# Kernel tuning notes

Hardware: AMD Instinct MI355X
Metric: run time of the kernel (lower is better)

## Reference

```python
import jax, jax.numpy as jnp
import numpy as np

NUM_CODES = 1024
CODE_DIM = 256
EMA_DECAY = 0.99
COMMITMENT = 0.25
EPS = 1e-6


def setup_inputs() -> dict:
    key = jax.random.key(0)
    k1, k2 = jax.random.split(key)
    z = jax.random.normal(k1, (64, 512, CODE_DIM), dtype=jnp.float32)
    embedding = jax.random.normal(k2, (NUM_CODES, CODE_DIM), dtype=jnp.float32)
    cluster_size = jnp.zeros((NUM_CODES,), dtype=jnp.float32)
    embedding_avg = embedding.copy()
    return {"z": z, "embedding": embedding, "cluster_size": cluster_size,
            "embedding_avg": embedding_avg}


def reference(z, embedding, cluster_size, embedding_avg):
    K, D = embedding.shape
    flat = z.reshape(-1, D)                                  # [N, D]
    dist = (jnp.sum(flat * flat, axis=1, keepdims=True)
            - 2.0 * (flat @ embedding.T)
            + jnp.sum(embedding * embedding, axis=1))
    indices = jnp.argmin(dist, axis=1)                       # [N]
    z_q = embedding[indices].reshape(z.shape)

    # EMA codebook update (training branch, no-grad in original)
    counts = jax.ops.segment_sum(jnp.ones_like(indices, dtype=flat.dtype),
                                 indices, num_segments=K)    # one-hot col sums
    embed_sum = jax.ops.segment_sum(flat, indices, num_segments=K)  # [K, D]
    new_cluster_size = cluster_size * EMA_DECAY + (1.0 - EMA_DECAY) * counts
    new_embedding_avg = embedding_avg * EMA_DECAY + (1.0 - EMA_DECAY) * embed_sum
    n = jnp.sum(new_cluster_size)
    cs = (new_cluster_size + EPS) / (n + K * EPS)
    new_embedding = new_embedding_avg / cs[:, None]

    loss = COMMITMENT * jnp.mean((jax.lax.stop_gradient(z_q) - z) ** 2)
    z_q_st = z + jax.lax.stop_gradient(z_q - z)
    return (z_q_st, loss, indices, new_cluster_size, new_embedding_avg,
            new_embedding)
```

## Files before the change

### kernel.cpp

```cpp
#include <hip/hip_runtime.h>

#define N_ROWS   32768
#define KCODES   1024
#define DDIM     256
#define RPB      64
#define NBLK     512

#define O_ZQ     0
#define O_LOSS   8388608
#define O_IDX    8388609
#define O_NCS    8421377
#define O_NEA    8422401
#define O_NEMB   8684545

#define W_ESUM   0
#define W_CNT    262144
#define W_ENORM  263168
#define W_LOSSP  264192
#define W_CUR    264704
#define W_N      265728
#define W_IDX    265792
#define W_SORT   298560

typedef _Float16 half_t;
typedef __attribute__((ext_vector_type(8))) _Float16 half8;
typedef __attribute__((ext_vector_type(4))) float floatx4;

__global__ __launch_bounds__(256)
void k_prep2(const float* __restrict__ emb, float* __restrict__ enorm,
             half_t* __restrict__ Bp, float* __restrict__ zero_ws) {
    __shared__ half_t hi[16 * 256];
    __shared__ half_t lo[16 * 256];
    __shared__ float  ssum[256];
    const int ct  = blockIdx.x;
    const int tid = threadIdx.x;
    const int c16 = tid >> 4;
    const int dp  = tid & 15;

    {
        float4 z4 = {0.f, 0.f, 0.f, 0.f};
        float4* wsf4 = (float4*)zero_ws;
        int t = ct * 256 + tid;
        #pragma unroll
        for (int i = 0; i < 4; ++i) wsf4[t + i * 16384] = z4;
        if (t < 256) wsf4[65536 + t] = z4;
    }

    float ss = 0.f;
    #pragma unroll
    for (int i = 0; i < 4; ++i) {
        float4 v = *(const float4*)(emb + (size_t)(ct * 16 + c16) * DDIM + dp * 16 + i * 4);
        ss += v.x * v.x + v.y * v.y + v.z * v.z + v.w * v.w;
        #pragma unroll
        for (int q = 0; q < 4; ++q) {
            float f = (&v.x)[q];
            half_t h = (half_t)f;
            hi[c16 * 256 + dp * 16 + i * 4 + q] = h;
            lo[c16 * 256 + dp * 16 + i * 4 + q] = (half_t)(f - (float)h);
        }
    }
    ssum[tid] = ss;
    __syncthreads();
    if (tid < 16) {
        float s = 0.f;
        #pragma unroll
        for (int i = 0; i < 16; ++i) s += ssum[tid * 16 + i];
        enorm[ct * 16 + tid] = s;
    }

    const int g16 = ((ct >> 4) << 2) | ((ct >> 2) & 3);
    const int ns  = ct & 3;
    #pragma unroll
    for (int i = 0; i < 4; ++i) {
        int f    = tid + i * 256;
        int ks   = f >> 6;
        int lane = f & 63;
        int cc   = lane & 15;
        int seg  = ks >> 3;
        int ko   = (ks & 7) * 32 + (lane >> 4) * 8;
        const half_t* src = (seg == 1) ? lo : hi;
        half8 v = *(const half8*)(src + cc * 256 + ko);
        *(half8*)(Bp + (((size_t)(g16 * 16 + ks) * 4 + ns) * 64 + lane) * 8) = v;
    }
}

__global__ __launch_bounds__(512)
void k_argmin(const float* __restrict__ z, const half_t* __restrict__ Bp,
              const float* __restrict__ enorm, const float* __restrict__ embf,
              int* __restrict__ out_idx, float* __restrict__ out_idx_f,
              float* __restrict__ out_zq, float* __restrict__ lossp,
              int* __restrict__ counts_i) {
    __shared__ __align__(16) half_t As[RPB * 512];

    const int tid  = threadIdx.x;
    const int w    = tid >> 6;
    const int lane = tid & 63;
    const int tx   = lane & 15;
    const int quad = lane >> 4;
    const int rh   = w >> 2;
    const int cq   = w & 3;
    const int rbase = blockIdx.x * RPB;

    #pragma unroll
    for (int it = 0; it < 4; ++it) {
        int f   = tid + it * 512;
        int row = f >> 5;
        int g   = f & 31;
        const float* zp = z + (size_t)(rbase + row) * DDIM + g * 8;
        float4 v0 = *(const float4*)zp;
        float4 v1 = *(const float4*)(zp + 4);
        half8 hi, lo;
        hi[0] = (half_t)v0.x; lo[0] = (half_t)(v0.x - (float)hi[0]);
        hi[1] = (half_t)v0.y; lo[1] = (half_t)(v0.y - (float)hi[1]);
        hi[2] = (half_t)v0.z; lo[2] = (half_t)(v0.z - (float)hi[2]);
        hi[3] = (half_t)v0.w; lo[3] = (half_t)(v0.w - (float)hi[3]);
        hi[4] = (half_t)v1.x; lo[4] = (half_t)(v1.x - (float)hi[4]);
        hi[5] = (half_t)v1.y; lo[5] = (half_t)(v1.y - (float)hi[5]);
        hi[6] = (half_t)v1.z; lo[6] = (half_t)(v1.z - (float)hi[6]);
        hi[7] = (half_t)v1.w; lo[7] = (half_t)(v1.w - (float)hi[7]);
        int sw = row & 7;
        *(half8*)(&As[row * 512 + ((g ^ sw)) * 8])        = hi;
        *(half8*)(&As[row * 512 + (((32 + g) ^ sw)) * 8]) = lo;
    }
    __syncthreads();

    floatx4 zero4 = {0.f, 0.f, 0.f, 0.f};
    float bd[2][4];
    int   bi[2][4];
    #pragma unroll
    for (int mt = 0; mt < 2; ++mt)
        #pragma unroll
        for (int r = 0; r < 4; ++r) { bd[mt][r] = 3.402823466e38f; bi[mt][r] = 0; }

    for (int g4 = 0; g4 < 4; ++g4) {
        const int cb = cq * 256 + g4 * 64;
        const half_t* Bg = Bp + (size_t)(cq * 4 + g4) * 32768 + (size_t)lane * 8;

        floatx4 acc[2][4];
        #pragma unroll
        for (int mt = 0; mt < 2; ++mt)
            #pragma unroll
            for (int ns = 0; ns < 4; ++ns) acc[mt][ns] = zero4;

        half8 B0[4], B1[4];
        #define LOADB(PK, BUF)                                                 \
            { const half_t* bp_ = Bg + (PK) * 2048;                            \
              _Pragma("unroll")                                                \
              for (int ns = 0; ns < 4; ++ns)                                   \
                  BUF[ns] = *(const half8*)(bp_ + ns * 512); }
        #define MFMA_BLK(BUF)                                                  \
            _Pragma("unroll")                                                  \
            for (int mt = 0; mt < 2; ++mt)                                     \
                _Pragma("unroll")                                              \
                for (int ns = 0; ns < 4; ++ns)                                 \
                    acc[mt][ns] = __builtin_amdgcn_mfma_f32_16x16x32_f16(      \
                        a[mt], BUF[ns], acc[mt][ns], 0, 0, 0);

        LOADB(0, B0);
        LOADB(1, B1);

        #pragma unroll 2
        for (int ks = 0; ks < 24; ++ks) {
            const int k8b = ((ks & 16) << 1) + (ks & 7) * 4;
            half8 a[2];
            #pragma unroll
            for (int mt = 0; mt < 2; ++mt) {
                int row = rh * 32 + mt * 16 + tx;
                a[mt] = *(half8*)(&As[row * 512 + ((k8b + quad) ^ (row & 7)) * 8]);
            }
            if (ks & 1) { MFMA_BLK(B1) } else { MFMA_BLK(B0) }
            if (ks + 2 < 24) {
                const int pkp = (ks + 2) & 15;
                if (ks & 1) { LOADB(pkp, B1); } else { LOADB(pkp, B0); }
            }
        }
        #undef LOADB
        #undef MFMA_BLK

        #pragma unroll
        for (int ns = 0; ns < 4; ++ns) {
            float en = enorm[cb + ns * 16 + tx];
            int   cc = cb + ns * 16 + tx;
            #pragma unroll
            for (int mt = 0; mt < 2; ++mt)
                #pragma unroll
                for (int r = 0; r < 4; ++r) {
                    float d = fmaf(-2.f, acc[mt][ns][r], en);
                    if (d < bd[mt][r]) { bd[mt][r] = d; bi[mt][r] = cc; }
                }
        }
    }

    #pragma unroll
    for (int mt = 0; mt < 2; ++mt)
        #pragma unroll
        for (int r = 0; r < 4; ++r) {
            float d = bd[mt][r];
            int   b = bi[mt][r];
            #pragma unroll
            for (int off = 8; off > 0; off >>= 1) {
                float od = __shfl_xor(d, off);
                int   ob = __shfl_xor(b, off);
                if (od < d || (od == d && ob < b)) { d = od; b = ob; }
            }
            bd[mt][r] = d; bi[mt][r] = b;
        }

    __syncthreads();
    float* sd   = (float*)As;
    int*   si   = ((int*)As) + 256;
    int*   sidx = ((int*)As) + 512;
    if (tx == 0) {
        #pragma unroll
        for (int mt = 0; mt < 2; ++mt)
            #pragma unroll
            for (int r = 0; r < 4; ++r) {
                int row = rh * 32 + mt * 16 + quad * 4 + r;
                sd[row * 4 + cq] = bd[mt][r];
                si[row * 4 + cq] = bi[mt][r];
            }
    }
    __syncthreads();
    if (tid < RPB) {
        int row = tid;
        float d = sd[row * 4];
        int   b = si[row * 4];
        #pragma unroll
        for (int ww = 1; ww < 4; ++ww) {
            float od = sd[row * 4 + ww];
            int   ob = si[row * 4 + ww];
            if (od < d || (od == d && ob < b)) { d = od; b = ob; }
        }
        sidx[row] = b;
        out_idx[rbase + row]   = b;
        out_idx_f[rbase + row] = (float)b;
        atomicAdd(&counts_i[b], 1);
    }
    __syncthreads();

    float l = 0.f;
    #pragma unroll
    for (int u = 0; u < 8; ++u) {
        int gi  = tid + u * 512;
        int row = gi >> 6;
        int c4  = gi & 63;
        int k   = sidx[row];
        float4 zv = *(const float4*)(z    + (size_t)(rbase + row) * DDIM + c4 * 4);
        float4 ev = *(const float4*)(embf + (size_t)k * DDIM + c4 * 4);
        float dx = ev.x - zv.x, dy = ev.y - zv.y, dz = ev.z - zv.z, dw = ev.w - zv.w;
        float4 o = { zv.x + dx, zv.y + dy, zv.z + dz, zv.w + dw };
        *(float4*)(out_zq + (size_t)(rbase + row) * DDIM + c4 * 4) = o;
        l += dx * dx + dy * dy + dz * dz + dw * dw;
    }
    #pragma unroll
    for (int off = 32; off > 0; off >>= 1) l += __shfl_down(l, off);
    __shared__ float ls[8];
    if (lane == 0) ls[w] = l;
    __syncthreads();
    if (tid == 0) {
        float s = 0.f;
        #pragma unroll
        for (int i = 0; i < 8; ++i) s += ls[i];
        lossp[blockIdx.x] = s;
    }
}

__global__ __launch_bounds__(256)
void k_scan(const float* __restrict__ cs_in, const int* __restrict__ counts_i,
            const float* __restrict__ lossp, float* __restrict__ out_ncs,
            int* __restrict__ cursors,
            float* __restrict__ n_out, float* __restrict__ loss_out) {
    const int tid = threadIdx.x;
    __shared__ int ps[256];
    int c[4]; int pt = 0;
    #pragma unroll
    for (int i = 0; i < 4; ++i) { c[i] = counts_i[tid * 4 + i]; pt += c[i]; }
    ps[tid] = pt;
    __syncthreads();
    for (int s = 1; s < 256; s <<= 1) {
        int v = (tid >= s) ? ps[tid - s] : 0;
        __syncthreads();
        ps[tid] += v;
        __syncthreads();
    }
    int o = ps[tid] - pt;
    float v = 0.f;
    #pragma unroll
    for (int i = 0; i < 4; ++i) {
        cursors[tid * 4 + i] = o;
        o += c[i];
        float nc = cs_in[tid * 4 + i] * 0.99f + 0.01f * (float)c[i];
        out_ncs[tid * 4 + i] = nc;
        v += nc;
    }
    float l = 0.f;
    for (int i = tid; i < NBLK; i += 256) l += lossp[i];
    #pragma unroll
    for (int off = 32; off > 0; off >>= 1) {
        v += __shfl_down(v, off);
        l += __shfl_down(l, off);
    }
    __shared__ float sv[4], sl[4];
    if ((tid & 63) == 0) { sv[tid >> 6] = v; sl[tid >> 6] = l; }
    __syncthreads();
    if (tid == 0) {
        n_out[0]    = sv[0] + sv[1] + sv[2] + sv[3];
        loss_out[0] = 0.25f * ((sl[0] + sl[1] + sl[2] + sl[3]) / 8388608.0f);
    }
}

__global__ __launch_bounds__(256)
void k_rank(const int* __restrict__ idx, int* __restrict__ cursors,
            int* __restrict__ rows_sorted) {
    int r = blockIdx.x * 256 + threadIdx.x;
    int k = idx[r];
    int pos = atomicAdd(&cursors[k], 1);
    rows_sorted[pos] = r;
}

__global__ __launch_bounds__(256)
void k_esum2(const float* __restrict__ z, const int* __restrict__ rows_sorted,
             const int* __restrict__ idx, float* __restrict__ esum) {
    const int tid  = threadIdx.x;
    const int w    = tid >> 6;
    const int lane = tid & 63;
    const int base = (blockIdx.x * 4 + w) * 32;

    int r = rows_sorted[base + (lane & 31)];
    int c = idx[r];
    float4 acc = {0.f, 0.f, 0.f, 0.f};
    #pragma unroll 8
    for (int j = 0; j < 32; ++j) {
        int rj = __shfl(r, j);
        int cj = __shfl(c, j);
        float4 zv = *(const float4*)(z + (size_t)rj * DDIM + lane * 4);
        acc.x += zv.x; acc.y += zv.y; acc.z += zv.z; acc.w += zv.w;
        int cn = (j < 31) ? __shfl(c, j + 1) : -1;
        if (cn != cj) {
            float* p = esum + (size_t)cj * DDIM + lane * 4;
            atomicAdd(p + 0, acc.x);
            atomicAdd(p + 1, acc.y);
            atomicAdd(p + 2, acc.z);
            atomicAdd(p + 3, acc.w);
            acc.x = 0.f; acc.y = 0.f; acc.z = 0.f; acc.w = 0.f;
        }
    }
}

__global__ __launch_bounds__(256)
void k_embed(const float* __restrict__ ea, const float* __restrict__ esum,
             const float* __restrict__ ncs, const float* __restrict__ n_ws,
             float* __restrict__ out_nea, float* __restrict__ out_nemb) {
    int k = blockIdx.x;
    int d = threadIdx.x;
    size_t off = (size_t)k * DDIM + d;
    float nea = ea[off] * 0.99f + 0.01f * esum[off];
    out_nea[off] = nea;
    float cs = (ncs[k] + 1e-6f) / (n_ws[0] + 0.001024f);
    out_nemb[off] = nea / cs;
}

extern "C" void kernel_launch(void* const* d_in, const int* in_sizes, int n_in,
                              void* d_out, int out_size, void* d_ws, size_t ws_size,
                              hipStream_t stream) {
    const float* z   = (const float*)d_in[0];
    const float* emb = (const float*)d_in[1];
    const float* cs  = (const float*)d_in[2];
    const float* ea  = (const float*)d_in[3];
    float* out = (float*)d_out;
    float* ws  = (float*)d_ws;

    float* esum    = ws + W_ESUM;
    int*   cnts    = (int*)(ws + W_CNT);
    float* enorm   = ws + W_ENORM;
    float* lossp   = ws + W_LOSSP;
    int*   curs    = (int*)(ws + W_CUR);
    float* wn      = ws + W_N;
    int*   widx    = (int*)(ws + W_IDX);
    int*   rsorted = (int*)(ws + W_SORT);

    half_t* Bp = (half_t*)(out + O_NEA + 3);

    k_prep2  <<<64, 256, 0, stream>>>(emb, enorm, Bp, ws);
    k_argmin <<<NBLK, 512, 0, stream>>>(z, Bp, enorm, emb,
                                        widx, out + O_IDX, out + O_ZQ, lossp, cnts);
    k_scan   <<<1, 256, 0, stream>>>(cs, cnts, lossp, out + O_NCS, curs,
                                     wn, out + O_LOSS);
    k_rank   <<<N_ROWS / 256, 256, 0, stream>>>(widx, curs, rsorted);
    k_esum2  <<<256, 256, 0, stream>>>(z, rsorted, widx, esum);
    k_embed  <<<KCODES, 256, 0, stream>>>(ea, esum, out + O_NCS, wn,
                                          out + O_NEA, out + O_NEMB);
}
```

Before: 202.1 us.

## Fuse scan, rank, esum and embed into one cooperative kernel

Merges the four post-argmin kernels into a single cooperative-launch kernel that uses grid syncs. Bucket ranks are now taken from the argmin counting atomics, which removes the separate rank pass, and the esum zeroing moves into the tail kernel. Two smaller changes ride along: the argmin kernel gets a remapped z staging load and triple-buffered B prefetch instead of double-buffered. The aim is to cut kernel launch gaps and the serial single-block scan, at the cost of grid-sync overhead and extra register pressure.

```diff
diff --git a/kernel.cpp b/kernel.cpp
--- a/kernel.cpp
+++ b/kernel.cpp
@@ -1,4 +1,7 @@
 #include <hip/hip_runtime.h>
+#include <hip/hip_cooperative_groups.h>
+
+namespace cg = cooperative_groups;
 
 #define N_ROWS   32768
 #define KCODES   1024
@@ -21,6 +24,7 @@
 #define W_N      265728
 #define W_IDX    265792
 #define W_SORT   298560
+#define W_RANK   331328
 
 typedef _Float16 half_t;
 typedef __attribute__((ext_vector_type(8))) _Float16 half8;
@@ -28,7 +32,7 @@
 
 __global__ __launch_bounds__(256)
 void k_prep2(const float* __restrict__ emb, float* __restrict__ enorm,
-             half_t* __restrict__ Bp, float* __restrict__ zero_ws) {
+             half_t* __restrict__ Bp, int* __restrict__ cnts) {
     __shared__ half_t hi[16 * 256];
     __shared__ half_t lo[16 * 256];
     __shared__ float  ssum[256];
@@ -37,13 +41,9 @@
     const int c16 = tid >> 4;
     const int dp  = tid & 15;
 
-    {
-        float4 z4 = {0.f, 0.f, 0.f, 0.f};
-        float4* wsf4 = (float4*)zero_ws;
-        int t = ct * 256 + tid;
-        #pragma unroll
-        for (int i = 0; i < 4; ++i) wsf4[t + i * 16384] = z4;
-        if (t < 256) wsf4[65536 + t] = z4;
+    if (ct == 0) {
+        int4 zz = {0, 0, 0, 0};
+        ((int4*)cnts)[tid] = zz;
     }
 
     float ss = 0.f;
@@ -89,7 +89,7 @@
               const float* __restrict__ enorm, const float* __restrict__ embf,
               int* __restrict__ out_idx, float* __restrict__ out_idx_f,
               float* __restrict__ out_zq, float* __restrict__ lossp,
-              int* __restrict__ counts_i) {
+              int* __restrict__ counts_i, int* __restrict__ rank_ws) {
     __shared__ __align__(16) half_t As[RPB * 512];
 
     const int tid  = threadIdx.x;
@@ -101,26 +101,27 @@
     const int cq   = w & 3;
     const int rbase = blockIdx.x * RPB;
 
-    #pragma unroll
-    for (int it = 0; it < 4; ++it) {
-        int f   = tid + it * 512;
-        int row = f >> 5;
-        int g   = f & 31;
-        const float* zp = z + (size_t)(rbase + row) * DDIM + g * 8;
-        float4 v0 = *(const float4*)zp;
-        float4 v1 = *(const float4*)(zp + 4);
-        half8 hi, lo;
-        hi[0] = (half_t)v0.x; lo[0] = (half_t)(v0.x - (float)hi[0]);
-        hi[1] = (half_t)v0.y; lo[1] = (half_t)(v0.y - (float)hi[1]);
-        hi[2] = (half_t)v0.z; lo[2] = (half_t)(v0.z - (float)hi[2]);
-        hi[3] = (half_t)v0.w; lo[3] = (half_t)(v0.w - (float)hi[3]);
-        hi[4] = (half_t)v1.x; lo[4] = (half_t)(v1.x - (float)hi[4]);
-        hi[5] = (half_t)v1.y; lo[5] = (half_t)(v1.y - (float)hi[5]);
-        hi[6] = (half_t)v1.z; lo[6] = (half_t)(v1.z - (float)hi[6]);
-        hi[7] = (half_t)v1.w; lo[7] = (half_t)(v1.w - (float)hi[7]);
-        int sw = row & 7;
-        *(half8*)(&As[row * 512 + ((g ^ sw)) * 8])        = hi;
-        *(half8*)(&As[row * 512 + (((32 + g) ^ sw)) * 8]) = lo;
+    {
+        const int arow = w * 8 + (lane >> 3);
+        const int sw   = arow & 7;
+        #pragma unroll
+        for (int it = 0; it < 4; ++it) {
+            int g = it * 8 + (lane & 7);
+            const float* zp = z + (size_t)(rbase + arow) * DDIM + g * 8;
+            float4 v0 = *(const float4*)zp;
+            float4 v1 = *(const float4*)(zp + 4);
+            half8 hi, lo;
+            hi[0] = (half_t)v0.x; lo[0] = (half_t)(v0.x - (float)hi[0]);
+            hi[1] = (half_t)v0.y; lo[1] = (half_t)(v0.y - (float)hi[1]);
+            hi[2] = (half_t)v0.z; lo[2] = (half_t)(v0.z - (float)hi[2]);
+            hi[3] = (half_t)v0.w; lo[3] = (half_t)(v0.w - (float)hi[3]);
+            hi[4] = (half_t)v1.x; lo[4] = (half_t)(v1.x - (float)hi[4]);
+            hi[5] = (half_t)v1.y; lo[5] = (half_t)(v1.y - (float)hi[5]);
+            hi[6] = (half_t)v1.z; lo[6] = (half_t)(v1.z - (float)hi[6]);
+            hi[7] = (half_t)v1.w; lo[7] = (half_t)(v1.w - (float)hi[7]);
+            *(half8*)(&As[arow * 512 + ((g ^ sw)) * 8])        = hi;
+            *(half8*)(&As[arow * 512 + (((32 + g) ^ sw)) * 8]) = lo;
+        }
     }
     __syncthreads();
 
@@ -142,7 +143,7 @@
             #pragma unroll
             for (int ns = 0; ns < 4; ++ns) acc[mt][ns] = zero4;
 
-        half8 B0[4], B1[4];
+        half8 B0[4], B1[4], B2[4];
         #define LOADB(PK, BUF)                                                 \
             { const half_t* bp_ = Bg + (PK) * 2048;                            \
               _Pragma("unroll")                                                \
@@ -158,8 +159,9 @@
 
         LOADB(0, B0);
         LOADB(1, B1);
-
-        #pragma unroll 2
+        LOADB(2, B2);
+
+        #pragma unroll 3
         for (int ks = 0; ks < 24; ++ks) {
             const int k8b = ((ks & 16) << 1) + (ks & 7) * 4;
             half8 a[2];
@@ -168,10 +170,16 @@
                 int row = rh * 32 + mt * 16 + tx;
                 a[mt] = *(half8*)(&As[row * 512 + ((k8b + quad) ^ (row & 7)) * 8]);
             }
-            if (ks & 1) { MFMA_BLK(B1) } else { MFMA_BLK(B0) }
-            if (ks + 2 < 24) {
-                const int pkp = (ks + 2) & 15;
-                if (ks & 1) { LOADB(pkp, B1); } else { LOADB(pkp, B0); }
+            const int m3 = ks % 3;
+            if (m3 == 0) {
+                MFMA_BLK(B0)
+                if (ks + 3 < 24) { LOADB((ks + 3) & 15, B0); }
+            } else if (m3 == 1) {
+                MFMA_BLK(B1)
+                if (ks + 3 < 24) { LOADB((ks + 3) & 15, B1); }
+            } else {
+                MFMA_BLK(B2)
+                if (ks + 3 < 24) { LOADB((ks + 3) & 15, B2); }
             }
         }
         #undef LOADB
@@ -234,7 +242,8 @@
         sidx[row] = b;
         out_idx[rbase + row]   = b;
         out_idx_f[rbase + row] = (float)b;
-        atomicAdd(&counts_i[b], 1);
+        int rk = atomicAdd(&counts_i[b], 1);
+        rank_ws[rbase + row] = rk;
     }
     __syncthreads();
 
@@ -266,12 +275,26 @@
 }
 
 __global__ __launch_bounds__(256)
-void k_scan(const float* __restrict__ cs_in, const int* __restrict__ counts_i,
-            const float* __restrict__ lossp, float* __restrict__ out_ncs,
-            int* __restrict__ cursors,
-            float* __restrict__ n_out, float* __restrict__ loss_out) {
+void k_tail(const float* __restrict__ cs_in, const int* __restrict__ counts_i,
+            const float* __restrict__ lossp, const int* __restrict__ idx,
+            const int* __restrict__ rank_ws, const float* __restrict__ z,
+            const float* __restrict__ ea,
+            float* __restrict__ out_ncs, float* __restrict__ n_ws,
+            float* __restrict__ loss_out, int* __restrict__ rows_sorted,
+            float* __restrict__ esum, float* __restrict__ out_nea,
+            float* __restrict__ out_nemb) {
+    cg::grid_group grid = cg::this_grid();
     const int tid = threadIdx.x;
+    const int bid = blockIdx.x;
+
     __shared__ int ps[256];
+    __shared__ int base_s[1024];
+    __shared__ float sv[4], sl[4];
+
+    {
+        float4 z4 = {0.f, 0.f, 0.f, 0.f};
+        ((float4*)esum)[bid * 256 + tid] = z4;
+    }
     int c[4]; int pt = 0;
     #pragma unroll
     for (int i = 0; i < 4; ++i) { c[i] = counts_i[tid * 4 + i]; pt += c[i]; }
@@ -287,77 +310,78 @@
     float v = 0.f;
     #pragma unroll
     for (int i = 0; i < 4; ++i) {
-        cursors[tid * 4 + i] = o;
+        base_s[tid * 4 + i] = o;
         o += c[i];
-        float nc = cs_in[tid * 4 + i] * 0.99f + 0.01f * (float)c[i];
-        out_ncs[tid * 4 + i] = nc;
-        v += nc;
-    }
-    float l = 0.f;
-    for (int i = tid; i < NBLK; i += 256) l += lossp[i];
-    #pragma unroll
-    for (int off = 32; off > 0; off >>= 1) {
-        v += __shfl_down(v, off);
-        l += __shfl_down(l, off);
-    }
-    __shared__ float sv[4], sl[4];
-    if ((tid & 63) == 0) { sv[tid >> 6] = v; sl[tid >> 6] = l; }
-    __syncthreads();
-    if (tid == 0) {
-        n_out[0]    = sv[0] + sv[1] + sv[2] + sv[3];
-        loss_out[0] = 0.25f * ((sl[0] + sl[1] + sl[2] + sl[3]) / 8388608.0f);
-    }
-}
-
-__global__ __launch_bounds__(256)
-void k_rank(const int* __restrict__ idx, int* __restrict__ cursors,
-            int* __restrict__ rows_sorted) {
-    int r = blockIdx.x * 256 + threadIdx.x;
-    int k = idx[r];
-    int pos = atomicAdd(&cursors[k], 1);
-    rows_sorted[pos] = r;
-}
-
-__global__ __launch_bounds__(256)
-void k_esum2(const float* __restrict__ z, const int* __restrict__ rows_sorted,
-             const int* __restrict__ idx, float* __restrict__ esum) {
-    const int tid  = threadIdx.x;
-    const int w    = tid >> 6;
-    const int lane = tid & 63;
-    const int base = (blockIdx.x * 4 + w) * 32;
-
-    int r = rows_sorted[base + (lane & 31)];
-    int c = idx[r];
-    float4 acc = {0.f, 0.f, 0.f, 0.f};
-    #pragma unroll 8
-    for (int j = 0; j < 32; ++j) {
-        int rj = __shfl(r, j);
-        int cj = __shfl(c, j);
-        float4 zv = *(const float4*)(z + (size_t)rj * DDIM + lane * 4);
-        acc.x += zv.x; acc.y += zv.y; acc.z += zv.z; acc.w += zv.w;
-        int cn = (j < 31) ? __shfl(c, j + 1) : -1;
-        if (cn != cj) {
-            float* p = esum + (size_t)cj * DDIM + lane * 4;
-            atomicAdd(p + 0, acc.x);
-            atomicAdd(p + 1, acc.y);
-            atomicAdd(p + 2, acc.z);
-            atomicAdd(p + 3, acc.w);
-            acc.x = 0.f; acc.y = 0.f; acc.z = 0.f; acc.w = 0.f;
-        }
-    }
-}
-
-__global__ __launch_bounds__(256)
-void k_embed(const float* __restrict__ ea, const float* __restrict__ esum,
-             const float* __restrict__ ncs, const float* __restrict__ n_ws,
-             float* __restrict__ out_nea, float* __restrict__ out_nemb) {
-    int k = blockIdx.x;
-    int d = threadIdx.x;
-    size_t off = (size_t)k * DDIM + d;
-    float nea = ea[off] * 0.99f + 0.01f * esum[off];
-    out_nea[off] = nea;
-    float cs = (ncs[k] + 1e-6f) / (n_ws[0] + 0.001024f);
-    out_nemb[off] = nea / cs;
+        if (bid == 0) {
+            float nc = cs_in[tid * 4 + i] * 0.99f + 0.01f * (float)c[i];
+            out_ncs[tid * 4 + i] = nc;
+            v += nc;
+        }
+    }
+    if (bid == 0) {
+        float l = 0.f;
+        for (int i = tid; i < NBLK; i += 256) l += lossp[i];
+        #pragma unroll
+        for (int off = 32; off > 0; off >>= 1) {
+            v += __shfl_down(v, off);
+            l += __shfl_down(l, off);
+        }
+        if ((tid & 63) == 0) { sv[tid >> 6] = v; sl[tid >> 6] = l; }
+        __syncthreads();
+        if (tid == 0) {
+            n_ws[0]     = sv[0] + sv[1] + sv[2] + sv[3];
+            loss_out[0] = 0.25f * ((sl[0] + sl[1] + sl[2] + sl[3]) / 8388608.0f);
+        }
+    }
+    __syncthreads();
+    if (tid < 128) {
+        int r = bid * 128 + tid;
+        int k = idx[r];
+        rows_sorted[base_s[k] + rank_ws[r]] = r;
+    }
+
+    grid.sync();
+
+    {
+        const int w    = tid >> 6;
+        const int lane = tid & 63;
+        const int base = (bid * 4 + w) * 32;
+        int r = rows_sorted[base + (lane & 31)];
+        int cc = idx[r];
+        float4 acc = {0.f, 0.f, 0.f, 0.f};
+        #pragma unroll 8
+        for (int j = 0; j < 32; ++j) {
+            int rj = __shfl(r, j);
+            int cj = __shfl(cc, j);
+            float4 zv = *(const float4*)(z + (size_t)rj * DDIM + lane * 4);
+            acc.x += zv.x; acc.y += zv.y; acc.z += zv.z; acc.w += zv.w;
+            int cn = (j < 31) ? __shfl(cc, j + 1) : -1;
+            if (cn != cj) {
+                float* p = esum + (size_t)cj * DDIM + lane * 4;
+                atomicAdd(p + 0, acc.x);
+                atomicAdd(p + 1, acc.y);
+                atomicAdd(p + 2, acc.z);
+                atomicAdd(p + 3, acc.w);
+                acc.x = 0.f; acc.y = 0.f; acc.z = 0.f; acc.w = 0.f;
+            }
+        }
+    }
+
+    grid.sync();
+
+    {
+        float nv = n_ws[0];
+        #pragma unroll
+        for (int i = 0; i < 4; ++i) {
+            int k = bid * 4 + i;
+            size_t off = (size_t)k * DDIM + tid;
+            float nea = ea[off] * 0.99f + 0.01f * esum[off];
+            out_nea[off] = nea;
+            float ncv = cs_in[k] * 0.99f + 0.01f * (float)counts_i[k];
+            float csv = (ncv + 1e-6f) / (nv + 0.001024f);
+            out_nemb[off] = nea / csv;
+        }
+    }
 }
 
 extern "C" void kernel_launch(void* const* d_in, const int* in_sizes, int n_in,
@@ -374,20 +398,28 @@
     int*   cnts    = (int*)(ws + W_CNT);
     float* enorm   = ws + W_ENORM;
     float* lossp   = ws + W_LOSSP;
-    int*   curs    = (int*)(ws + W_CUR);
     float* wn      = ws + W_N;
     int*   widx    = (int*)(ws + W_IDX);
     int*   rsorted = (int*)(ws + W_SORT);
+    int*   rankw   = (int*)(ws + W_RANK);
 
     half_t* Bp = (half_t*)(out + O_NEA + 3);
 
-    k_prep2  <<<64, 256, 0, stream>>>(emb, enorm, Bp, ws);
+    k_prep2  <<<64, 256, 0, stream>>>(emb, enorm, Bp, cnts);
     k_argmin <<<NBLK, 512, 0, stream>>>(z, Bp, enorm, emb,
-                                        widx, out + O_IDX, out + O_ZQ, lossp, cnts);
-    k_scan   <<<1, 256, 0, stream>>>(cs, cnts, lossp, out + O_NCS, curs,
-                                     wn, out + O_LOSS);
-    k_rank   <<<N_ROWS / 256, 256, 0, stream>>>(widx, curs, rsorted);
-    k_esum2  <<<256, 256, 0, stream>>>(z, rsorted, widx, esum);
-    k_embed  <<<KCODES, 256, 0, stream>>>(ea, esum, out + O_NCS, wn,
-                                          out + O_NEA, out + O_NEMB);
+                                        widx, out + O_IDX, out + O_ZQ, lossp,
+                                        cnts, rankw);
+
+    float* o_ncs  = out + O_NCS;
+    float* o_loss = out + O_LOSS;
+    float* o_nea  = out + O_NEA;
+    float* o_nemb = out + O_NEMB;
+    void* args[] = {
+        (void*)&cs, (void*)&cnts, (void*)&lossp, (void*)&widx, (void*)&rankw,
+        (void*)&z, (void*)&ea,
+        (void*)&o_ncs, (void*)&wn, (void*)&o_loss, (void*)&rsorted,
+        (void*)&esum, (void*)&o_nea, (void*)&o_nemb
+    };
+    hipLaunchCooperativeKernel((const void*)k_tail, dim3(256), dim3(256),
+                               args, 0, stream);
 }
```

Result: slower. 260.2 us (+28.8%).

## Fuse EMA tail into one atomic-free per-code gather kernel and restructure argmin k-loop

Applied to the files above, without the earlier changes.

Replaces the scan, rank, atomic segment-sum and embed kernels with a single kernel. Each block owns four codes, scans all indices to build a shared-memory list of its rows, and accumulates the z rows in registers without global atomics. This removes three launches and the zeroing of the large esum workspace. The argmin k-loop is also restructured to load the hi and lo A fragments together against the same B buffer, and the A staging is remapped to whole-row ownership per wave. The cost is that every block rereads the full index array, and rows are gathered with little parallelism when a code is popular.

```diff
diff --git a/kernel.cpp b/kernel.cpp
--- a/kernel.cpp
+++ b/kernel.cpp
@@ -13,14 +13,10 @@
 #define O_NEA    8422401
 #define O_NEMB   8684545
 
-#define W_ESUM   0
 #define W_CNT    262144
 #define W_ENORM  263168
 #define W_LOSSP  264192
-#define W_CUR    264704
-#define W_N      265728
 #define W_IDX    265792
-#define W_SORT   298560
 
 typedef _Float16 half_t;
 typedef __attribute__((ext_vector_type(8))) _Float16 half8;
@@ -28,7 +24,7 @@
 
 __global__ __launch_bounds__(256)
 void k_prep2(const float* __restrict__ emb, float* __restrict__ enorm,
-             half_t* __restrict__ Bp, float* __restrict__ zero_ws) {
+             half_t* __restrict__ Bp, int* __restrict__ cnts) {
     __shared__ half_t hi[16 * 256];
     __shared__ half_t lo[16 * 256];
     __shared__ float  ssum[256];
@@ -37,13 +33,9 @@
     const int c16 = tid >> 4;
     const int dp  = tid & 15;
 
-    {
-        float4 z4 = {0.f, 0.f, 0.f, 0.f};
-        float4* wsf4 = (float4*)zero_ws;
-        int t = ct * 256 + tid;
-        #pragma unroll
-        for (int i = 0; i < 4; ++i) wsf4[t + i * 16384] = z4;
-        if (t < 256) wsf4[65536 + t] = z4;
+    if (ct == 0) {
+        int4 zz = {0, 0, 0, 0};
+        ((int4*)cnts)[tid] = zz;
     }
 
     float ss = 0.f;
@@ -101,26 +93,27 @@
     const int cq   = w & 3;
     const int rbase = blockIdx.x * RPB;
 
-    #pragma unroll
-    for (int it = 0; it < 4; ++it) {
-        int f   = tid + it * 512;
-        int row = f >> 5;
-        int g   = f & 31;
-        const float* zp = z + (size_t)(rbase + row) * DDIM + g * 8;
-        float4 v0 = *(const float4*)zp;
-        float4 v1 = *(const float4*)(zp + 4);
-        half8 hi, lo;
-        hi[0] = (half_t)v0.x; lo[0] = (half_t)(v0.x - (float)hi[0]);
-        hi[1] = (half_t)v0.y; lo[1] = (half_t)(v0.y - (float)hi[1]);
-        hi[2] = (half_t)v0.z; lo[2] = (half_t)(v0.z - (float)hi[2]);
-        hi[3] = (half_t)v0.w; lo[3] = (half_t)(v0.w - (float)hi[3]);
-        hi[4] = (half_t)v1.x; lo[4] = (half_t)(v1.x - (float)hi[4]);
-        hi[5] = (half_t)v1.y; lo[5] = (half_t)(v1.y - (float)hi[5]);
-        hi[6] = (half_t)v1.z; lo[6] = (half_t)(v1.z - (float)hi[6]);
-        hi[7] = (half_t)v1.w; lo[7] = (half_t)(v1.w - (float)hi[7]);
-        int sw = row & 7;
-        *(half8*)(&As[row * 512 + ((g ^ sw)) * 8])        = hi;
-        *(half8*)(&As[row * 512 + (((32 + g) ^ sw)) * 8]) = lo;
+    {
+        const int arow = w * 8 + (lane >> 3);
+        const int sw   = arow & 7;
+        #pragma unroll
+        for (int it = 0; it < 4; ++it) {
+            int g = it * 8 + (lane & 7);
+            const float* zp = z + (size_t)(rbase + arow) * DDIM + g * 8;
+            float4 v0 = *(const float4*)zp;
+            float4 v1 = *(const float4*)(zp + 4);
+            half8 hi, lo;
+            hi[0] = (half_t)v0.x; lo[0] = (half_t)(v0.x - (float)hi[0]);
+            hi[1] = (half_t)v0.y; lo[1] = (half_t)(v0.y - (float)hi[1]);
+            hi[2] = (half_t)v0.z; lo[2] = (half_t)(v0.z - (float)hi[2]);
+            hi[3] = (half_t)v0.w; lo[3] = (half_t)(v0.w - (float)hi[3]);
+            hi[4] = (half_t)v1.x; lo[4] = (half_t)(v1.x - (float)hi[4]);
+            hi[5] = (half_t)v1.y; lo[5] = (half_t)(v1.y - (float)hi[5]);
+            hi[6] = (half_t)v1.z; lo[6] = (half_t)(v1.z - (float)hi[6]);
+            hi[7] = (half_t)v1.w; lo[7] = (half_t)(v1.w - (float)hi[7]);
+            *(half8*)(&As[arow * 512 + ((g ^ sw)) * 8])        = hi;
+            *(half8*)(&As[arow * 512 + (((32 + g) ^ sw)) * 8]) = lo;
+        }
     }
     __syncthreads();
 
@@ -148,31 +141,41 @@
               _Pragma("unroll")                                                \
               for (int ns = 0; ns < 4; ++ns)                                   \
                   BUF[ns] = *(const half8*)(bp_ + ns * 512); }
-        #define MFMA_BLK(BUF)                                                  \
+        #define MFMA_BLK(AF, BUF)                                              \
             _Pragma("unroll")                                                  \
             for (int mt = 0; mt < 2; ++mt)                                     \
                 _Pragma("unroll")                                              \
                 for (int ns = 0; ns < 4; ++ns)                                 \
                     acc[mt][ns] = __builtin_amdgcn_mfma_f32_16x16x32_f16(      \
-                        a[mt], BUF[ns], acc[mt][ns], 0, 0, 0);
+                        AF[mt], BUF[ns], acc[mt][ns], 0, 0, 0);
 
         LOADB(0, B0);
         LOADB(1, B1);
 
         #pragma unroll 2
-        for (int ks = 0; ks < 24; ++ks) {
-            const int k8b = ((ks & 16) << 1) + (ks & 7) * 4;
-            half8 a[2];
+        for (int s = 0; s < 8; ++s) {
+            half8 a0[2], a1[2];
             #pragma unroll
             for (int mt = 0; mt < 2; ++mt) {
                 int row = rh * 32 + mt * 16 + tx;
-                a[mt] = *(half8*)(&As[row * 512 + ((k8b + quad) ^ (row & 7)) * 8]);
+                int sw  = row & 7;
+                a0[mt] = *(half8*)(&As[row * 512 + ((s * 4 + quad) ^ sw) * 8]);
+                a1[mt] = *(half8*)(&As[row * 512 + ((32 + s * 4 + quad) ^ sw) * 8]);
             }
-            if (ks & 1) { MFMA_BLK(B1) } else { MFMA_BLK(B0) }
-            if (ks + 2 < 24) {
-                const int pkp = (ks + 2) & 15;
-                if (ks & 1) { LOADB(pkp, B1); } else { LOADB(pkp, B0); }
+            if (s & 1) { MFMA_BLK(a0, B1) MFMA_BLK(a1, B1) LOADB(s + 2, B1); }
+            else       { MFMA_BLK(a0, B0) MFMA_BLK(a1, B0) LOADB(s + 2, B0); }
+        }
+        #pragma unroll 2
+        for (int s = 8; s < 16; ++s) {
+            half8 a0[2];
+            #pragma unroll
+            for (int mt = 0; mt < 2; ++mt) {
+                int row = rh * 32 + mt * 16 + tx;
+                int sw  = row & 7;
+                a0[mt] = *(half8*)(&As[row * 512 + (((s - 8) * 4 + quad) ^ sw) * 8]);
             }
+            if (s & 1) { MFMA_BLK(a0, B1) if (s + 2 < 16) LOADB(s + 2, B1); }
+            else       { MFMA_BLK(a0, B0) if (s + 2 < 16) LOADB(s + 2, B0); }
         }
         #undef LOADB
         #undef MFMA_BLK
@@ -266,98 +269,101 @@
 }
 
 __global__ __launch_bounds__(256)
-void k_scan(const float* __restrict__ cs_in, const int* __restrict__ counts_i,
-            const float* __restrict__ lossp, float* __restrict__ out_ncs,
-            int* __restrict__ cursors,
-            float* __restrict__ n_out, float* __restrict__ loss_out) {
-    const int tid = threadIdx.x;
-    __shared__ int ps[256];
-    int c[4]; int pt = 0;
-    #pragma unroll
-    for (int i = 0; i < 4; ++i) { c[i] = counts_i[tid * 4 + i]; pt += c[i]; }
-    ps[tid] = pt;
-    __syncthreads();
-    for (int s = 1; s < 256; s <<= 1) {
-        int v = (tid >= s) ? ps[tid - s] : 0;
-        __syncthreads();
-        ps[tid] += v;
-        __syncthreads();
-    }
-    int o = ps[tid] - pt;
-    float v = 0.f;
-    #pragma unroll
-    for (int i = 0; i < 4; ++i) {
-        cursors[tid * 4 + i] = o;
-        o += c[i];
-        float nc = cs_in[tid * 4 + i] * 0.99f + 0.01f * (float)c[i];
-        out_ncs[tid * 4 + i] = nc;
-        v += nc;
-    }
-    float l = 0.f;
-    for (int i = tid; i < NBLK; i += 256) l += lossp[i];
-    #pragma unroll
-    for (int off = 32; off > 0; off >>= 1) {
-        v += __shfl_down(v, off);
-        l += __shfl_down(l, off);
-    }
-    __shared__ float sv[4], sl[4];
-    if ((tid & 63) == 0) { sv[tid >> 6] = v; sl[tid >> 6] = l; }
-    __syncthreads();
-    if (tid == 0) {
-        n_out[0]    = sv[0] + sv[1] + sv[2] + sv[3];
-        loss_out[0] = 0.25f * ((sl[0] + sl[1] + sl[2] + sl[3]) / 8388608.0f);
-    }
-}
-
-__global__ __launch_bounds__(256)
-void k_rank(const int* __restrict__ idx, int* __restrict__ cursors,
-            int* __restrict__ rows_sorted) {
-    int r = blockIdx.x * 256 + threadIdx.x;
-    int k = idx[r];
-    int pos = atomicAdd(&cursors[k], 1);
-    rows_sorted[pos] = r;
-}
-
-__global__ __launch_bounds__(256)
-void k_esum2(const float* __restrict__ z, const int* __restrict__ rows_sorted,
-             const int* __restrict__ idx, float* __restrict__ esum) {
+void k_tail2(const float* __restrict__ cs_in, const int* __restrict__ counts_i,
+             const float* __restrict__ lossp, const int* __restrict__ idx,
+             const float* __restrict__ z, const float* __restrict__ ea,
+             float* __restrict__ out_ncs, float* __restrict__ loss_out,
+             float* __restrict__ out_nea, float* __restrict__ out_nemb) {
     const int tid  = threadIdx.x;
+    const int bid  = blockIdx.x;
+    const int kb   = bid * 4;
     const int w    = tid >> 6;
     const int lane = tid & 63;
-    const int base = (blockIdx.x * 4 + w) * 32;
-
-    int r = rows_sorted[base + (lane & 31)];
-    int c = idx[r];
-    float4 acc = {0.f, 0.f, 0.f, 0.f};
-    #pragma unroll 8
-    for (int j = 0; j < 32; ++j) {
-        int rj = __shfl(r, j);
-        int cj = __shfl(c, j);
-        float4 zv = *(const float4*)(z + (size_t)rj * DDIM + lane * 4);
-        acc.x += zv.x; acc.y += zv.y; acc.z += zv.z; acc.w += zv.w;
-        int cn = (j < 31) ? __shfl(c, j + 1) : -1;
-        if (cn != cj) {
-            float* p = esum + (size_t)cj * DDIM + lane * 4;
-            atomicAdd(p + 0, acc.x);
-            atomicAdd(p + 1, acc.y);
-            atomicAdd(p + 2, acc.z);
-            atomicAdd(p + 3, acc.w);
-            acc.x = 0.f; acc.y = 0.f; acc.z = 0.f; acc.w = 0.f;
-        }
-    }
-}
-
-__global__ __launch_bounds__(256)
-void k_embed(const float* __restrict__ ea, const float* __restrict__ esum,
-             const float* __restrict__ ncs, const float* __restrict__ n_ws,
-             float* __restrict__ out_nea, float* __restrict__ out_nemb) {
-    int k = blockIdx.x;
-    int d = threadIdx.x;
-    size_t off = (size_t)k * DDIM + d;
-    float nea = ea[off] * 0.99f + 0.01f * esum[off];
-    out_nea[off] = nea;
-    float cs = (ncs[k] + 1e-6f) / (n_ws[0] + 0.001024f);
-    out_nemb[off] = nea / cs;
+
+    __shared__ int    list[4096];
+    __shared__ int    lcnt;
+    __shared__ float4 accW[4][4][64];
+    __shared__ float  snv[4], slv[4];
+
+    float pn = 0.f;
+    #pragma unroll
+    for (int i = 0; i < 4; ++i) {
+        int c = tid * 4 + i;
+        float nc = cs_in[c] * 0.99f + 0.01f * (float)counts_i[c];
+        pn += nc;
+        if (bid == 0) out_ncs[c] = nc;
+    }
+    float pl = (bid == 0) ? (lossp[tid] + lossp[tid + 256]) : 0.f;
+    #pragma unroll
+    for (int off = 32; off > 0; off >>= 1) {
+        pn += __shfl_down(pn, off);
+        pl += __shfl_down(pl, off);
+    }
+    if (lane == 0) { snv[w] = pn; slv[w] = pl; }
+    __syncthreads();
+    const float nval = snv[0] + snv[1] + snv[2] + snv[3];
+    if (bid == 0 && tid == 0)
+        loss_out[0] = 0.25f * ((slv[0] + slv[1] + slv[2] + slv[3]) / 8388608.0f);
+
+    float4 a0 = {0.f,0.f,0.f,0.f}, a1 = a0, a2 = a0, a3 = a0;
+    for (int ch = 0; ch < 8; ++ch) {
+        __syncthreads();
+        if (tid == 0) lcnt = 0;
+        __syncthreads();
+        const int4* ip = (const int4*)(idx + ch * 4096);
+        #pragma unroll
+        for (int i = 0; i < 4; ++i) {
+            int4 v = ip[tid + i * 256];
+            int r0 = ch * 4096 + (tid + i * 256) * 4;
+            int d;
+            d = v.x - kb; if ((unsigned)d < 4u) { int p = atomicAdd(&lcnt, 1); list[p] = r0 | (d << 15); }
+            d = v.y - kb; if ((unsigned)d < 4u) { int p = atomicAdd(&lcnt, 1); list[p] = (r0 + 1) | (d << 15); }
+            d = v.z - kb; if ((unsigned)d < 4u) { int p = atomicAdd(&lcnt, 1); list[p] = (r0 + 2) | (d << 15); }
+            d = v.w - kb; if ((unsigned)d < 4u) { int p = atomicAdd(&lcnt, 1); list[p] = (r0 + 3) | (d << 15); }
+        }
+        __syncthreads();
+        const int n = lcnt;
+        for (int i = w; i < n; i += 4) {
+            int packed = list[i];
+            int row = packed & 32767;
+            int lc  = packed >> 15;
+            float4 v = *((const float4*)(z + (size_t)row * DDIM) + lane);
+            if      (lc == 0) { a0.x += v.x; a0.y += v.y; a0.z += v.z; a0.w += v.w; }
+            else if (lc == 1) { a1.x += v.x; a1.y += v.y; a1.z += v.z; a1.w += v.w; }
+            else if (lc == 2) { a2.x += v.x; a2.y += v.y; a2.z += v.z; a2.w += v.w; }
+            else              { a3.x += v.x; a3.y += v.y; a3.z += v.z; a3.w += v.w; }
+        }
+    }
+    __syncthreads();
+    accW[0][w][lane] = a0;
+    accW[1][w][lane] = a1;
+    accW[2][w][lane] = a2;
+    accW[3][w][lane] = a3;
+    __syncthreads();
+
+    {
+        const int c = tid >> 6;
+        const int l = tid & 63;
+        float4 e0 = accW[c][0][l];
+        float4 e1 = accW[c][1][l];
+        float4 e2 = accW[c][2][l];
+        float4 e3 = accW[c][3][l];
+        float ex = e0.x + e1.x + e2.x + e3.x;
+        float ey = e0.y + e1.y + e2.y + e3.y;
+        float ez = e0.z + e1.z + e2.z + e3.z;
+        float ew = e0.w + e1.w + e2.w + e3.w;
+        size_t off = (size_t)(kb + c) * DDIM + l * 4;
+        float4 av = *(const float4*)(ea + off);
+        float4 nea = { av.x * 0.99f + 0.01f * ex,
+                       av.y * 0.99f + 0.01f * ey,
+                       av.z * 0.99f + 0.01f * ez,
+                       av.w * 0.99f + 0.01f * ew };
+        *(float4*)(out_nea + off) = nea;
+        float ncv = cs_in[kb + c] * 0.99f + 0.01f * (float)counts_i[kb + c];
+        float csv = (ncv + 1e-6f) / (nval + 0.001024f);
+        float4 nemb = { nea.x / csv, nea.y / csv, nea.z / csv, nea.w / csv };
+        *(float4*)(out_nemb + off) = nemb;
+    }
 }
 
 extern "C" void kernel_launch(void* const* d_in, const int* in_sizes, int n_in,
@@ -370,24 +376,18 @@
     float* out = (float*)d_out;
     float* ws  = (float*)d_ws;
 
-    float* esum    = ws + W_ESUM;
     int*   cnts    = (int*)(ws + W_CNT);
     float* enorm   = ws + W_ENORM;
     float* lossp   = ws + W_LOSSP;
-    int*   curs    = (int*)(ws + W_CUR);
-    float* wn      = ws + W_N;
     int*   widx    = (int*)(ws + W_IDX);
-    int*   rsorted = (int*)(ws + W_SORT);
 
     half_t* Bp = (half_t*)(out + O_NEA + 3);
 
-    k_prep2  <<<64, 256, 0, stream>>>(emb, enorm, Bp, ws);
+    k_prep2  <<<64, 256, 0, stream>>>(emb, enorm, Bp, cnts);
     k_argmin <<<NBLK, 512, 0, stream>>>(z, Bp, enorm, emb,
-                                        widx, out + O_IDX, out + O_ZQ, lossp, cnts);
-    k_scan   <<<1, 256, 0, stream>>>(cs, cnts, lossp, out + O_NCS, curs,
-                                     wn, out + O_LOSS);
-    k_rank   <<<N_ROWS / 256, 256, 0, stream>>>(widx, curs, rsorted);
-    k_esum2  <<<256, 256, 0, stream>>>(z, rsorted, widx, esum);
-    k_embed  <<<KCODES, 256, 0, stream>>>(ea, esum, out + O_NCS, wn,
-                                          out + O_NEA, out + O_NEMB);
+                                        widx, out + O_IDX, out + O_ZQ, lossp,
+                                        cnts);
+    k_tail2  <<<256, 256, 0, stream>>>(cs, cnts, lossp, widx, z, ea,
+                                       out + O_NCS, out + O_LOSS,
+                                       out + O_NEA, out + O_NEMB);
 }
```

Result: slower. 270.0 us (+33.6%).

## Fuse scan and rank into one scatter kernel, reuse A fragments in argmin

Applied to the files above, without the earlier changes.

The argmin kernel now records each row's atomic rank within its code bucket. That lets a new multi-block scatter kernel compute prefix offsets per block and place rows without a second round of atomics, merging the single-block scan and the rank kernel into one launch. The MFMA K-loop is restructured to load B fragments for 16 steps instead of 24 and reuse them across hi and lo A halves, and the z staging loop is remapped per warp. The embed kernel is vectorised to float4 with 4 codes per block. The trade-off is that every block redundantly recomputes the 1024-entry prefix scan, and the rank buffer costs extra workspace.

```diff
diff --git a/kernel.cpp b/kernel.cpp
--- a/kernel.cpp
+++ b/kernel.cpp
@@ -17,10 +17,10 @@
 #define W_CNT    262144
 #define W_ENORM  263168
 #define W_LOSSP  264192
-#define W_CUR    264704
 #define W_N      265728
 #define W_IDX    265792
 #define W_SORT   298560
+#define W_RANK   331328
 
 typedef _Float16 half_t;
 typedef __attribute__((ext_vector_type(8))) _Float16 half8;
@@ -89,7 +89,7 @@
               const float* __restrict__ enorm, const float* __restrict__ embf,
               int* __restrict__ out_idx, float* __restrict__ out_idx_f,
               float* __restrict__ out_zq, float* __restrict__ lossp,
-              int* __restrict__ counts_i) {
+              int* __restrict__ counts_i, int* __restrict__ rank_ws) {
     __shared__ __align__(16) half_t As[RPB * 512];
 
     const int tid  = threadIdx.x;
@@ -101,26 +101,27 @@
     const int cq   = w & 3;
     const int rbase = blockIdx.x * RPB;
 
-    #pragma unroll
-    for (int it = 0; it < 4; ++it) {
-        int f   = tid + it * 512;
-        int row = f >> 5;
-        int g   = f & 31;
-        const float* zp = z + (size_t)(rbase + row) * DDIM + g * 8;
-        float4 v0 = *(const float4*)zp;
-        float4 v1 = *(const float4*)(zp + 4);
-        half8 hi, lo;
-        hi[0] = (half_t)v0.x; lo[0] = (half_t)(v0.x - (float)hi[0]);
-        hi[1] = (half_t)v0.y; lo[1] = (half_t)(v0.y - (float)hi[1]);
-        hi[2] = (half_t)v0.z; lo[2] = (half_t)(v0.z - (float)hi[2]);
-        hi[3] = (half_t)v0.w; lo[3] = (half_t)(v0.w - (float)hi[3]);
-        hi[4] = (half_t)v1.x; lo[4] = (half_t)(v1.x - (float)hi[4]);
-        hi[5] = (half_t)v1.y; lo[5] = (half_t)(v1.y - (float)hi[5]);
-        hi[6] = (half_t)v1.z; lo[6] = (half_t)(v1.z - (float)hi[6]);
-        hi[7] = (half_t)v1.w; lo[7] = (half_t)(v1.w - (float)hi[7]);
-        int sw = row & 7;
-        *(half8*)(&As[row * 512 + ((g ^ sw)) * 8])        = hi;
-        *(half8*)(&As[row * 512 + (((32 + g) ^ sw)) * 8]) = lo;
+    {
+        const int arow = w * 8 + (lane >> 3);
+        const int sw   = arow & 7;
+        #pragma unroll
+        for (int it = 0; it < 4; ++it) {
+            int g = it * 8 + (lane & 7);
+            const float* zp = z + (size_t)(rbase + arow) * DDIM + g * 8;
+            float4 v0 = *(const float4*)zp;
+            float4 v1 = *(const float4*)(zp + 4);
+            half8 hi, lo;
+            hi[0] = (half_t)v0.x; lo[0] = (half_t)(v0.x - (float)hi[0]);
+            hi[1] = (half_t)v0.y; lo[1] = (half_t)(v0.y - (float)hi[1]);
+            hi[2] = (half_t)v0.z; lo[2] = (half_t)(v0.z - (float)hi[2]);
+            hi[3] = (half_t)v0.w; lo[3] = (half_t)(v0.w - (float)hi[3]);
+            hi[4] = (half_t)v1.x; lo[4] = (half_t)(v1.x - (float)hi[4]);
+            hi[5] = (half_t)v1.y; lo[5] = (half_t)(v1.y - (float)hi[5]);
+            hi[6] = (half_t)v1.z; lo[6] = (half_t)(v1.z - (float)hi[6]);
+            hi[7] = (half_t)v1.w; lo[7] = (half_t)(v1.w - (float)hi[7]);
+            *(half8*)(&As[arow * 512 + ((g ^ sw)) * 8])        = hi;
+            *(half8*)(&As[arow * 512 + (((32 + g) ^ sw)) * 8]) = lo;
+        }
     }
     __syncthreads();
 
@@ -148,31 +149,41 @@
               _Pragma("unroll")                                                \
               for (int ns = 0; ns < 4; ++ns)                                   \
                   BUF[ns] = *(const half8*)(bp_ + ns * 512); }
-        #define MFMA_BLK(BUF)                                                  \
+        #define MFMA_BLK(AF, BUF)                                              \
             _Pragma("unroll")                                                  \
             for (int mt = 0; mt < 2; ++mt)                                     \
                 _Pragma("unroll")                                              \
                 for (int ns = 0; ns < 4; ++ns)                                 \
                     acc[mt][ns] = __builtin_amdgcn_mfma_f32_16x16x32_f16(      \
-                        a[mt], BUF[ns], acc[mt][ns], 0, 0, 0);
+                        AF[mt], BUF[ns], acc[mt][ns], 0, 0, 0);
 
         LOADB(0, B0);
         LOADB(1, B1);
 
         #pragma unroll 2
-        for (int ks = 0; ks < 24; ++ks) {
-            const int k8b = ((ks & 16) << 1) + (ks & 7) * 4;
-            half8 a[2];
+        for (int s = 0; s < 8; ++s) {
+            half8 a0[2], a1[2];
             #pragma unroll
             for (int mt = 0; mt < 2; ++mt) {
                 int row = rh * 32 + mt * 16 + tx;
-                a[mt] = *(half8*)(&As[row * 512 + ((k8b + quad) ^ (row & 7)) * 8]);
+                int sw  = row & 7;
+                a0[mt] = *(half8*)(&As[row * 512 + ((s * 4 + quad) ^ sw) * 8]);
+                a1[mt] = *(half8*)(&As[row * 512 + ((32 + s * 4 + quad) ^ sw) * 8]);
             }
-            if (ks & 1) { MFMA_BLK(B1) } else { MFMA_BLK(B0) }
-            if (ks + 2 < 24) {
-                const int pkp = (ks + 2) & 15;
-                if (ks & 1) { LOADB(pkp, B1); } else { LOADB(pkp, B0); }
+            if (s & 1) { MFMA_BLK(a0, B1) MFMA_BLK(a1, B1) LOADB(s + 2, B1); }
+            else       { MFMA_BLK(a0, B0) MFMA_BLK(a1, B0) LOADB(s + 2, B0); }
+        }
+        #pragma unroll 2
+        for (int s = 8; s < 16; ++s) {
+            half8 a0[2];
+            #pragma unroll
+            for (int mt = 0; mt < 2; ++mt) {
+                int row = rh * 32 + mt * 16 + tx;
+                int sw  = row & 7;
+                a0[mt] = *(half8*)(&As[row * 512 + (((s - 8) * 4 + quad) ^ sw) * 8]);
             }
+            if (s & 1) { MFMA_BLK(a0, B1) if (s + 2 < 16) LOADB(s + 2, B1); }
+            else       { MFMA_BLK(a0, B0) if (s + 2 < 16) LOADB(s + 2, B0); }
         }
         #undef LOADB
         #undef MFMA_BLK
@@ -234,7 +245,8 @@
         sidx[row] = b;
         out_idx[rbase + row]   = b;
         out_idx_f[rbase + row] = (float)b;
-        atomicAdd(&counts_i[b], 1);
+        int rk = atomicAdd(&counts_i[b], 1);
+        rank_ws[rbase + row] = rk;
     }
     __syncthreads();
 
@@ -266,12 +278,17 @@
 }
 
 __global__ __launch_bounds__(256)
-void k_scan(const float* __restrict__ cs_in, const int* __restrict__ counts_i,
-            const float* __restrict__ lossp, float* __restrict__ out_ncs,
-            int* __restrict__ cursors,
-            float* __restrict__ n_out, float* __restrict__ loss_out) {
+void k_scatter(const float* __restrict__ cs_in, const int* __restrict__ counts_i,
+               const float* __restrict__ lossp, const int* __restrict__ idx,
+               const int* __restrict__ rank_ws, int* __restrict__ rows_sorted,
+               float* __restrict__ out_ncs, float* __restrict__ n_ws,
+               float* __restrict__ loss_out) {
     const int tid = threadIdx.x;
+    const int bid = blockIdx.x;
     __shared__ int ps[256];
+    __shared__ int base_s[1024];
+    __shared__ float sv[4], sl[4];
+
     int c[4]; int pt = 0;
     #pragma unroll
     for (int i = 0; i < 4; ++i) { c[i] = counts_i[tid * 4 + i]; pt += c[i]; }
@@ -287,35 +304,31 @@
     float v = 0.f;
     #pragma unroll
     for (int i = 0; i < 4; ++i) {
-        cursors[tid * 4 + i] = o;
+        base_s[tid * 4 + i] = o;
         o += c[i];
-        float nc = cs_in[tid * 4 + i] * 0.99f + 0.01f * (float)c[i];
-        out_ncs[tid * 4 + i] = nc;
-        v += nc;
-    }
-    float l = 0.f;
-    for (int i = tid; i < NBLK; i += 256) l += lossp[i];
-    #pragma unroll
-    for (int off = 32; off > 0; off >>= 1) {
-        v += __shfl_down(v, off);
-        l += __shfl_down(l, off);
-    }
-    __shared__ float sv[4], sl[4];
-    if ((tid & 63) == 0) { sv[tid >> 6] = v; sl[tid >> 6] = l; }
-    __syncthreads();
-    if (tid == 0) {
-        n_out[0]    = sv[0] + sv[1] + sv[2] + sv[3];
+        if (bid == 0) {
+            float nc = cs_in[tid * 4 + i] * 0.99f + 0.01f * (float)c[i];
+            out_ncs[tid * 4 + i] = nc;
+            v += nc;
+        }
+    }
+    if (bid == 0) {
+        float l = lossp[tid] + lossp[tid + 256];
+        #pragma unroll
+        for (int off = 32; off > 0; off >>= 1) {
+            v += __shfl_down(v, off);
+            l += __shfl_down(l, off);
+        }
+        if ((tid & 63) == 0) { sv[tid >> 6] = v; sl[tid >> 6] = l; }
+    }
+    __syncthreads();
+    if (bid == 0 && tid == 0) {
+        n_ws[0]     = sv[0] + sv[1] + sv[2] + sv[3];
         loss_out[0] = 0.25f * ((sl[0] + sl[1] + sl[2] + sl[3]) / 8388608.0f);
     }
-}
-
-__global__ __launch_bounds__(256)
-void k_rank(const int* __restrict__ idx, int* __restrict__ cursors,
-            int* __restrict__ rows_sorted) {
-    int r = blockIdx.x * 256 + threadIdx.x;
+    int r = bid * 256 + tid;
     int k = idx[r];
-    int pos = atomicAdd(&cursors[k], 1);
-    rows_sorted[pos] = r;
+    rows_sorted[base_s[k] + rank_ws[r]] = r;
 }
 
 __global__ __launch_bounds__(256)
@@ -351,13 +364,21 @@
 void k_embed(const float* __restrict__ ea, const float* __restrict__ esum,
              const float* __restrict__ ncs, const float* __restrict__ n_ws,
              float* __restrict__ out_nea, float* __restrict__ out_nemb) {
-    int k = blockIdx.x;
-    int d = threadIdx.x;
-    size_t off = (size_t)k * DDIM + d;
-    float nea = ea[off] * 0.99f + 0.01f * esum[off];
-    out_nea[off] = nea;
-    float cs = (ncs[k] + 1e-6f) / (n_ws[0] + 0.001024f);
-    out_nemb[off] = nea / cs;
+    const int tid = threadIdx.x;
+    const int kb  = blockIdx.x * 4;
+    const int c   = tid >> 6;
+    const int l   = tid & 63;
+    size_t off = (size_t)(kb + c) * DDIM + l * 4;
+    float4 av = *(const float4*)(ea   + off);
+    float4 ev = *(const float4*)(esum + off);
+    float4 nea = { av.x * 0.99f + 0.01f * ev.x,
+                   av.y * 0.99f + 0.01f * ev.y,
+                   av.z * 0.99f + 0.01f * ev.z,
+                   av.w * 0.99f + 0.01f * ev.w };
+    *(float4*)(out_nea + off) = nea;
+    float csv = (ncs[kb + c] + 1e-6f) / (n_ws[0] + 0.001024f);
+    float4 nemb = { nea.x / csv, nea.y / csv, nea.z / csv, nea.w / csv };
+    *(float4*)(out_nemb + off) = nemb;
 }
 
 extern "C" void kernel_launch(void* const* d_in, const int* in_sizes, int n_in,
@@ -374,20 +395,20 @@
     int*   cnts    = (int*)(ws + W_CNT);
     float* enorm   = ws + W_ENORM;
     float* lossp   = ws + W_LOSSP;
-    int*   curs    = (int*)(ws + W_CUR);
     float* wn      = ws + W_N;
     int*   widx    = (int*)(ws + W_IDX);
     int*   rsorted = (int*)(ws + W_SORT);
+    int*   rankw   = (int*)(ws + W_RANK);
 
     half_t* Bp = (half_t*)(out + O_NEA + 3);
 
-    k_prep2  <<<64, 256, 0, stream>>>(emb, enorm, Bp, ws);
-    k_argmin <<<NBLK, 512, 0, stream>>>(z, Bp, enorm, emb,
-                                        widx, out + O_IDX, out + O_ZQ, lossp, cnts);
-    k_scan   <<<1, 256, 0, stream>>>(cs, cnts, lossp, out + O_NCS, curs,
-                                     wn, out + O_LOSS);
-    k_rank   <<<N_ROWS / 256, 256, 0, stream>>>(widx, curs, rsorted);
-    k_esum2  <<<256, 256, 0, stream>>>(z, rsorted, widx, esum);
-    k_embed  <<<KCODES, 256, 0, stream>>>(ea, esum, out + O_NCS, wn,
-                                          out + O_NEA, out + O_NEMB);
-}
+    k_prep2   <<<64, 256, 0, stream>>>(emb, enorm, Bp, ws);
+    k_argmin  <<<NBLK, 512, 0, stream>>>(z, Bp, enorm, emb,
+                                         widx, out + O_IDX, out + O_ZQ, lossp,
+                                         cnts, rankw);
+    k_scatter <<<128, 256, 0, stream>>>(cs, cnts, lossp, widx, rankw, rsorted,
+                                        out + O_NCS, wn, out + O_LOSS);
+    k_esum2   <<<256, 256, 0, stream>>>(z, rsorted, widx, esum);
+    k_embed   <<<256, 256, 0, stream>>>(ea, esum, out + O_NCS, wn,
+                                        out + O_NEA, out + O_NEMB);
+}
```

Measured after the change: 179.8 us, median of 3. -11.0%, faster.
